# Kernel optimization log

Measured on AMD Instinct MI355X. Metric: run time of the kernel, lower is better.

The kernel has to match this reference:

```python
import jax, jax.numpy as jnp
import numpy as np

EPS = 1e-5
K = 20


def _edge_layer(feat, W, g, b, k):
    # feat: (B, N, C). Dynamic KNN in feature space (DGCNN get_graph_feature).
    B = feat.shape[0]
    inner = jnp.einsum('bnc,bmc->bnm', feat, feat)          # (B,N,N)
    xx = jnp.sum(feat * feat, axis=-1)                      # (B,N)
    neg_dist = 2.0 * inner - xx[:, :, None] - xx[:, None, :]
    idx = jax.lax.top_k(neg_dist, k)[1]                     # (B,N,k) nearest (incl self)
    nbr = feat[jnp.arange(B)[:, None, None], idx]           # (B,N,k,C) gather
    ctr = jnp.broadcast_to(feat[:, :, None, :], nbr.shape)
    edge = jnp.concatenate([nbr - ctr, ctr], axis=-1)       # (B,N,k,2C)
    h = jnp.einsum('bnke,oe->bnko', edge, W)                # 1x1 conv
    mean = jnp.mean(h, axis=(0, 1, 2))
    var = jnp.var(h, axis=(0, 1, 2))                        # biased, as torch BN training
    h = (h - mean) * jax.lax.rsqrt(var + EPS) * g + b
    h = jax.nn.leaky_relu(h, 0.2)
    return jnp.max(h, axis=2)                               # max over k -> (B,N,C)


def setup_inputs() -> dict:
    key = jax.random.key(0)
    ks = jax.random.split(key, 8)
    B, N, C, OUT = 16, 2048, 64, 1024
    d = {
        'x': jax.random.normal(ks[0], (B, N, C), jnp.float32),
        'W1': jax.random.normal(ks[1], (C, 2 * C), jnp.float32) * 0.05,
        'g1': jnp.ones((C,), jnp.float32), 'b1': jnp.zeros((C,), jnp.float32),
        'W2': jax.random.normal(ks[2], (C, 2 * C), jnp.float32) * 0.05,
        'g2': jnp.ones((C,), jnp.float32), 'b2': jnp.zeros((C,), jnp.float32),
        'W3': jax.random.normal(ks[3], (C, 2 * C), jnp.float32) * 0.05,
        'g3': jnp.ones((C,), jnp.float32), 'b3': jnp.zeros((C,), jnp.float32),
        'Wf': jax.random.normal(ks[4], (OUT, 3 * C), jnp.float32) * 0.05,
        'gf': jnp.ones((OUT,), jnp.float32), 'bf': jnp.zeros((OUT,), jnp.float32),
    }
    return d


def reference(x, W1, g1, b1, W2, g2, b2, W3, g3, b3, Wf, gf, bf):
    # x: (B, N, C)
    f1 = _edge_layer(x, W1, g1, b1, K)
    f2 = _edge_layer(f1, W2, g2, b2, K)
    f3 = _edge_layer(f2, W3, g3, b3, K)
    cat = jnp.concatenate([f1, f2, f3], axis=-1)            # (B,N,3C)
    h = jnp.einsum('bnc,oc->bno', cat, Wf)                  # 1x1 conv1d
    mean = jnp.mean(h, axis=(0, 1))
    var = jnp.var(h, axis=(0, 1))
    h = (h - mean) * jax.lax.rsqrt(var + EPS) * gf + bf
    h = jax.nn.leaky_relu(h, 0.2)
    return jnp.max(h, axis=1)                               # global max over N -> (B,OUT)
```

## Files before the change

kernel.cpp:

```cpp
#include <hip/hip_runtime.h>

#define BB 16
#define NN 2048
#define CC 64
#define KNN 20
#define OUTC 1024

__global__ __launch_bounds__(256) void xx32_kernel(const float* __restrict__ F,
                                                   float* __restrict__ xxf) {
  int p = blockIdx.x * 256 + threadIdx.x;
  const float* f = F + (size_t)p * CC;
  float t[64];
#pragma unroll
  for (int c = 0; c < 64; ++c) t[c] = f[c] * f[c];
  float r[8];
#pragma unroll
  for (int j = 0; j < 8; ++j) r[j] = t[j];
#pragma unroll
  for (int i = 8; i < 64; i += 8)
#pragma unroll
    for (int j = 0; j < 8; ++j) r[j] += t[i + j];
  float res = ((r[0] + r[1]) + (r[2] + r[3])) + ((r[4] + r[5]) + (r[6] + r[7]));
  xxf[p] = res;
}

__device__ __forceinline__ unsigned long long packkey(float s, int m) {
  unsigned int u = __float_as_uint(s);
  u ^= (u >> 31) ? 0xFFFFFFFFu : 0x80000000u;
  return ((unsigned long long)u << 32) | (unsigned int)(NN - 1 - m);
}

#define INSERT_KEY(key)                                   \
  if ((key) > kv[KNN - 1]) {                              \
    _Pragma("unroll")                                     \
    for (int jj = KNN - 1; jj >= 1; --jj) {               \
      if ((key) > kv[jj - 1]) kv[jj] = kv[jj - 1];        \
      else if ((key) > kv[jj]) kv[jj] = (key);            \
    }                                                     \
    if ((key) > kv[0]) kv[0] = (key);                     \
  }

__global__ __launch_bounds__(256) void knn_fast(const float* __restrict__ F,
                                                const float* __restrict__ xxf,
                                                int* __restrict__ idx) {
  __shared__ __align__(16) char smem[52736];
  float* SQc = (float*)smem;
  float* SPc = (float*)(smem + 17408);
  float* SS  = (float*)(smem + 34816);
  float* xq  = (float*)(smem + 52224);
  float* xp  = (float*)(smem + 52480);

  int b = blockIdx.y, n0 = blockIdx.x * 64, t = threadIdx.x;
  const float* fb = F + (size_t)b * NN * CC;

#pragma unroll
  for (int j = 0; j < 4; ++j) {
    int v = t + 256 * j;
    int row = v >> 4, c4 = (v & 15) * 4;
    float4 val = *(const float4*)(fb + (size_t)(n0 + row) * CC + c4);
    SQc[(c4 + 0) * 68 + row] = val.x;
    SQc[(c4 + 1) * 68 + row] = val.y;
    SQc[(c4 + 2) * 68 + row] = val.z;
    SQc[(c4 + 3) * 68 + row] = val.w;
  }
  if (t < 64) xq[t] = xxf[b * NN + n0 + t];

  unsigned long long kv[KNN];
#pragma unroll
  for (int k = 0; k < KNN; ++k) kv[k] = 0ull;

  int tx = t & 15, ty = t >> 4;
  int r = t & 63, qq = t >> 6;

  for (int m0 = 0; m0 < NN; m0 += 64) {
    __syncthreads();
#pragma unroll
    for (int j = 0; j < 4; ++j) {
      int v = t + 256 * j;
      int row = v >> 4, c4 = (v & 15) * 4;
      float4 val = *(const float4*)(fb + (size_t)(m0 + row) * CC + c4);
      SPc[(c4 + 0) * 68 + row] = val.x;
      SPc[(c4 + 1) * 68 + row] = val.y;
      SPc[(c4 + 2) * 68 + row] = val.z;
      SPc[(c4 + 3) * 68 + row] = val.w;
    }
    if (t < 64) xp[t] = xxf[b * NN + m0 + t];
    __syncthreads();

    float acc[4][4] = {};
#pragma unroll 8
    for (int c = 0; c < 64; ++c) {
      float4 av = *(const float4*)&SQc[c * 68 + ty * 4];
      float4 bv = *(const float4*)&SPc[c * 68 + tx * 4];
      float a[4] = {av.x, av.y, av.z, av.w};
      float bb4[4] = {bv.x, bv.y, bv.z, bv.w};
#pragma unroll
      for (int i = 0; i < 4; ++i)
#pragma unroll
        for (int j = 0; j < 4; ++j) acc[i][j] = fmaf(a[i], bb4[j], acc[i][j]);
    }
#pragma unroll
    for (int i = 0; i < 4; ++i) {
      float xn = xq[ty * 4 + i];
      float4 sv;
      sv.x = (2.0f * acc[i][0] - xn) - xp[tx * 4 + 0];
      sv.y = (2.0f * acc[i][1] - xn) - xp[tx * 4 + 1];
      sv.z = (2.0f * acc[i][2] - xn) - xp[tx * 4 + 2];
      sv.w = (2.0f * acc[i][3] - xn) - xp[tx * 4 + 3];
      *(float4*)&SS[(ty * 4 + i) * 68 + tx * 4] = sv;
    }
    __syncthreads();

#pragma unroll
    for (int j4 = 0; j4 < 4; ++j4) {
      float4 sv = *(const float4*)&SS[r * 68 + qq * 16 + j4 * 4];
      int mb = m0 + qq * 16 + j4 * 4;
      unsigned long long k0 = packkey(sv.x, mb + 0);
      INSERT_KEY(k0)
      unsigned long long k1 = packkey(sv.y, mb + 1);
      INSERT_KEY(k1)
      unsigned long long k2 = packkey(sv.z, mb + 2);
      INSERT_KEY(k2)
      unsigned long long k3 = packkey(sv.w, mb + 3);
      INSERT_KEY(k3)
    }
  }

  __syncthreads();
  unsigned long long* keys = (unsigned long long*)smem;
#pragma unroll
  for (int k = 0; k < KNN; ++k) keys[t * KNN + k] = kv[k];
  __syncthreads();
  if (t < 64) {
    for (int q2 = 1; q2 < 4; ++q2) {
      int base = (q2 * 64 + t) * KNN;
#pragma unroll 1
      for (int k = 0; k < KNN; ++k) {
        unsigned long long key = keys[base + k];
        if (key <= kv[KNN - 1]) break;
        INSERT_KEY(key)
      }
    }
    int* dst = idx + (size_t)(b * NN + n0 + t) * KNN;
#pragma unroll
    for (int k = 0; k < KNN; ++k)
      dst[k] = (NN - 1) - (int)(unsigned int)(kv[k] & 0xFFFFFFFFull);
  }
}

template <int CACHE>
__global__ __launch_bounds__(256) void stats_k(const float* __restrict__ F,
                                               const float* __restrict__ W,
                                               const int* __restrict__ idx,
                                               double* __restrict__ sums,
                                               float* __restrict__ hout) {
  __shared__ float Fn[64 * 64];
  __shared__ double rs[256], rss[256];
  int b = blockIdx.y, n0 = blockIdx.x * 64, t = threadIdx.x;
  int o = t & 63, g4 = t >> 6;
#pragma unroll
  for (int j = 0; j < 4; ++j) {
    int v = t + 256 * j;
    int row = v >> 4, c4 = (v & 15) * 4;
    *(float4*)&Fn[row * 64 + c4] =
        *(const float4*)(F + ((size_t)(b * NN + n0 + row)) * CC + c4);
  }
  float4 w0[16], w1[16];
  const float* wp = W + o * 128;
#pragma unroll
  for (int c4 = 0; c4 < 16; ++c4) {
    w0[c4] = *(const float4*)(wp + c4 * 4);
    w1[c4] = *(const float4*)(wp + 64 + c4 * 4);
  }
  __syncthreads();
  double s = 0.0, ss = 0.0;
  for (int i = 0; i < 16; ++i) {
    int n = n0 + g4 * 16 + i;
    float4 fn[16];
#pragma unroll
    for (int c4 = 0; c4 < 16; ++c4) fn[c4] = *(float4*)&Fn[(g4 * 16 + i) * 64 + c4 * 4];
    const int* ip = idx + ((size_t)(b * NN + n)) * KNN;
#pragma unroll 1
    for (int k = 0; k < KNN; k += 2) {
      const float* fp0 = F + ((size_t)(b * NN + ip[k])) * CC;
      const float* fp1 = F + ((size_t)(b * NN + ip[k + 1])) * CC;
      float a0 = 0.f, a1 = 0.f;
#pragma unroll
      for (int c4 = 0; c4 < 16; ++c4) {
        float4 f0 = *(const float4*)(fp0 + c4 * 4);
        float4 f1 = *(const float4*)(fp1 + c4 * 4);
        float4 fv = fn[c4], wv = w0[c4];
        a0 = fmaf(wv.x, f0.x - fv.x, a0);
        a0 = fmaf(wv.y, f0.y - fv.y, a0);
        a0 = fmaf(wv.z, f0.z - fv.z, a0);
        a0 = fmaf(wv.w, f0.w - fv.w, a0);
        a1 = fmaf(wv.x, f1.x - fv.x, a1);
        a1 = fmaf(wv.y, f1.y - fv.y, a1);
        a1 = fmaf(wv.z, f1.z - fv.z, a1);
        a1 = fmaf(wv.w, f1.w - fv.w, a1);
      }
#pragma unroll
      for (int c4 = 0; c4 < 16; ++c4) {
        float4 fv = fn[c4], wv = w1[c4];
        a0 = fmaf(wv.x, fv.x, a0);
        a0 = fmaf(wv.y, fv.y, a0);
        a0 = fmaf(wv.z, fv.z, a0);
        a0 = fmaf(wv.w, fv.w, a0);
        a1 = fmaf(wv.x, fv.x, a1);
        a1 = fmaf(wv.y, fv.y, a1);
        a1 = fmaf(wv.z, fv.z, a1);
        a1 = fmaf(wv.w, fv.w, a1);
      }
      s += (double)a0 + (double)a1;
      ss += (double)a0 * (double)a0 + (double)a1 * (double)a1;
      if (CACHE) {
        float* hp = hout + (((size_t)(b * NN + n)) * KNN + k) * 64 + o;
        hp[0] = a0;
        hp[64] = a1;
      }
    }
  }
  rs[t] = s; rss[t] = ss;
  __syncthreads();
  if (t < 64) {
    double a = rs[t] + rs[t + 64] + rs[t + 128] + rs[t + 192];
    double q = rss[t] + rss[t + 64] + rss[t + 128] + rss[t + 192];
    atomicAdd(&sums[o], a);
    atomicAdd(&sums[64 + o], q);
  }
}

__global__ void finalize_np(const double* __restrict__ sums, double cntinv,
                            float* __restrict__ mrs) {
  int c = threadIdx.x;
  double mean = sums[c] * cntinv;
  double var = sums[64 + c] * cntinv - mean * mean;
  mrs[c] = (float)mean;
  mrs[64 + c] = 1.0f / sqrtf((float)var + 1e-5f);
}

__global__ __launch_bounds__(256) void apply_cached(const float* __restrict__ hin,
                                                    const float* __restrict__ mrs,
                                                    const float* __restrict__ gv,
                                                    const float* __restrict__ bvv,
                                                    float* __restrict__ Fo) {
  int t = threadIdx.x;
  int o = t & 63, ng = t >> 6;
  size_t n = (size_t)blockIdx.x * 4 + ng;
  const float* hp = hin + n * KNN * 64 + o;
  float m32 = mrs[o], rs32 = mrs[64 + o];
  float gg = gv[o], bb = bvv[o];
  float mx = -3.0e38f;
#pragma unroll
  for (int k = 0; k < KNN; ++k) {
    float h = hp[k * 64];
    float d = h - m32;
    d = d * rs32;
    d = d * gg;
    float y = d + bb;
    y = y >= 0.f ? y : 0.2f * y;
    mx = fmaxf(mx, y);
  }
  Fo[n * 64 + o] = mx;
}

__global__ __launch_bounds__(256) void apply_rec(const float* __restrict__ F,
                                                 const float* __restrict__ W,
                                                 const int* __restrict__ idx,
                                                 const float* __restrict__ mrs,
                                                 const float* __restrict__ gv,
                                                 const float* __restrict__ bvv,
                                                 float* __restrict__ Fo) {
  __shared__ float Fn[64 * 64];
  int b = blockIdx.y, n0 = blockIdx.x * 64, t = threadIdx.x;
  int o = t & 63, g4 = t >> 6;
#pragma unroll
  for (int j = 0; j < 4; ++j) {
    int v = t + 256 * j;
    int row = v >> 4, c4 = (v & 15) * 4;
    *(float4*)&Fn[row * 64 + c4] =
        *(const float4*)(F + ((size_t)(b * NN + n0 + row)) * CC + c4);
  }
  float4 w0[16], w1[16];
  const float* wp = W + o * 128;
#pragma unroll
  for (int c4 = 0; c4 < 16; ++c4) {
    w0[c4] = *(const float4*)(wp + c4 * 4);
    w1[c4] = *(const float4*)(wp + 64 + c4 * 4);
  }
  __syncthreads();
  float m32 = mrs[o], rs32 = mrs[64 + o];
  float gg = gv[o], bb = bvv[o];
  for (int i = 0; i < 16; ++i) {
    int n = n0 + g4 * 16 + i;
    float4 fn[16];
#pragma unroll
    for (int c4 = 0; c4 < 16; ++c4) fn[c4] = *(float4*)&Fn[(g4 * 16 + i) * 64 + c4 * 4];
    const int* ip = idx + ((size_t)(b * NN + n)) * KNN;
    float mx = -3.0e38f;
#pragma unroll 1
    for (int k = 0; k < KNN; k += 2) {
      const float* fp0 = F + ((size_t)(b * NN + ip[k])) * CC;
      const float* fp1 = F + ((size_t)(b * NN + ip[k + 1])) * CC;
      float a0 = 0.f, a1 = 0.f;
#pragma unroll
      for (int c4 = 0; c4 < 16; ++c4) {
        float4 f0 = *(const float4*)(fp0 + c4 * 4);
        float4 f1 = *(const float4*)(fp1 + c4 * 4);
        float4 fv = fn[c4], wv = w0[c4];
        a0 = fmaf(wv.x, f0.x - fv.x, a0);
        a0 = fmaf(wv.y, f0.y - fv.y, a0);
        a0 = fmaf(wv.z, f0.z - fv.z, a0);
        a0 = fmaf(wv.w, f0.w - fv.w, a0);
        a1 = fmaf(wv.x, f1.x - fv.x, a1);
        a1 = fmaf(wv.y, f1.y - fv.y, a1);
        a1 = fmaf(wv.z, f1.z - fv.z, a1);
        a1 = fmaf(wv.w, f1.w - fv.w, a1);
      }
#pragma unroll
      for (int c4 = 0; c4 < 16; ++c4) {
        float4 fv = fn[c4], wv = w1[c4];
        a0 = fmaf(wv.x, fv.x, a0);
        a0 = fmaf(wv.y, fv.y, a0);
        a0 = fmaf(wv.z, fv.z, a0);
        a0 = fmaf(wv.w, fv.w, a0);
        a1 = fmaf(wv.x, fv.x, a1);
        a1 = fmaf(wv.y, fv.y, a1);
        a1 = fmaf(wv.z, fv.z, a1);
        a1 = fmaf(wv.w, fv.w, a1);
      }
      float d0 = a0 - m32; d0 = d0 * rs32; d0 = d0 * gg;
      float y0 = d0 + bb;
      y0 = y0 >= 0.f ? y0 : 0.2f * y0;
      float d1 = a1 - m32; d1 = d1 * rs32; d1 = d1 * gg;
      float y1 = d1 + bb;
      y1 = y1 >= 0.f ? y1 : 0.2f * y1;
      mx = fmaxf(mx, fmaxf(y0, y1));
    }
    Fo[((size_t)(b * NN + n)) * CC + o] = mx;
  }
}

template <int CACHE>
__global__ __launch_bounds__(256) void fstats_split(const float* __restrict__ F1,
                                                    const float* __restrict__ F2,
                                                    const float* __restrict__ F3,
                                                    const float* __restrict__ Wf,
                                                    double* __restrict__ sums,
                                                    float* __restrict__ hout) {
  __shared__ float Wl[64 * 193];
  __shared__ double rs[256], rss[256];
  int b = blockIdx.y, o0 = blockIdx.x * 64, t = threadIdx.x;
  int nbase = blockIdx.z * (NN / 8);
  for (int j = 0; j < 48; ++j) {
    int v = t + 256 * j;
    int oo = v / 192, c = v - oo * 192;
    Wl[oo * 193 + c] = Wf[(size_t)(o0 + oo) * 192 + c];
  }
  __syncthreads();
  int o = t & 63, g = t >> 6;
  const float* fs[3] = {F1, F2, F3};
  double s = 0.0, ss = 0.0;
  for (int n0 = nbase; n0 < nbase + NN / 8; n0 += 16) {
    int n = n0 + g * 4;
    float h[4] = {0.f, 0.f, 0.f, 0.f};
#pragma unroll
    for (int part = 0; part < 3; ++part) {
      const float* src = fs[part] + ((size_t)(b * NN + n)) * CC;
      const float* wp = &Wl[o * 193 + part * 64];
#pragma unroll 4
      for (int c4 = 0; c4 < 16; ++c4) {
        float4 w4 = {wp[c4 * 4], wp[c4 * 4 + 1], wp[c4 * 4 + 2], wp[c4 * 4 + 3]};
#pragma unroll
        for (int i = 0; i < 4; ++i) {
          float4 v = *(const float4*)(src + (size_t)i * CC + c4 * 4);
          h[i] = fmaf(w4.x, v.x, h[i]);
          h[i] = fmaf(w4.y, v.y, h[i]);
          h[i] = fmaf(w4.z, v.z, h[i]);
          h[i] = fmaf(w4.w, v.w, h[i]);
        }
      }
    }
#pragma unroll
    for (int i = 0; i < 4; ++i) {
      s += (double)h[i];
      ss += (double)h[i] * (double)h[i];
      if (CACHE) hout[((size_t)(b * NN + n + i)) * OUTC + o0 + o] = h[i];
    }
  }
  rs[t] = s; rss[t] = ss;
  __syncthreads();
  if (t < 64) {
    double a = rs[t] + rs[t + 64] + rs[t + 128] + rs[t + 192];
    double q = rss[t] + rss[t + 64] + rss[t + 128] + rss[t + 192];
    atomicAdd(&sums[o0 + o], a);
    atomicAdd(&sums[1024 + o0 + o], q);
  }
}

__global__ void finalize_f(const double* __restrict__ sums,
                           const float* __restrict__ g,
                           const float* __restrict__ bb, double cntinv,
                           float* __restrict__ scsh) {
  int c = blockIdx.x * 256 + threadIdx.x;
  double mean = sums[c] * cntinv;
  double var = sums[1024 + c] * cntinv - mean * mean;
  double sc = (double)g[c] / sqrt(var + 1e-5);
  scsh[c] = (float)sc;
  scsh[1024 + c] = (float)((double)bb[c] - mean * sc);
}

__global__ __launch_bounds__(256) void fapply_stream(const float* __restrict__ hin,
                                                     const float* __restrict__ scsh,
                                                     float* __restrict__ pmax) {
  int b = blockIdx.y, t = threadIdx.x;
  int o = blockIdx.x * 256 + t;
  int nbase = blockIdx.z * (NN / 8);
  float sc = scsh[o], sh = scsh[1024 + o];
  float mx = -3.0e38f;
  const float* hp = hin + ((size_t)(b * NN + nbase)) * OUTC + o;
#pragma unroll 4
  for (int n = 0; n < NN / 8; ++n) {
    float y = fmaf(sc, hp[(size_t)n * OUTC], sh);
    y = y >= 0.f ? y : 0.2f * y;
    mx = fmaxf(mx, y);
  }
  pmax[((size_t)blockIdx.z * BB + b) * OUTC + o] = mx;
}

__global__ __launch_bounds__(256) void freduce(const float* __restrict__ pmax,
                                               float* __restrict__ out) {
  int v = blockIdx.x * 256 + threadIdx.x;
  float mx = -3.0e38f;
#pragma unroll
  for (int ch = 0; ch < 8; ++ch) mx = fmaxf(mx, pmax[(size_t)ch * BB * OUTC + v]);
  out[v] = mx;
}

__global__ __launch_bounds__(256) void fapply32(const float* __restrict__ F1,
                                                const float* __restrict__ F2,
                                                const float* __restrict__ F3,
                                                const float* __restrict__ Wf,
                                                const float* __restrict__ scsh,
                                                float* __restrict__ out) {
  __shared__ float Wl[64 * 193];
  __shared__ float redm[4][64];
  int b = blockIdx.y, o0 = blockIdx.x * 64, t = threadIdx.x;
  for (int j = 0; j < 48; ++j) {
    int v = t + 256 * j;
    int oo = v / 192, c = v - oo * 192;
    Wl[oo * 193 + c] = Wf[(size_t)(o0 + oo) * 192 + c];
  }
  __syncthreads();
  int o = t & 63, g = t >> 6;
  float sc = scsh[o0 + o], sh = scsh[1024 + o0 + o];
  const float* fs[3] = {F1, F2, F3};
  float mx = -3.0e38f;
  for (int n0 = 0; n0 < NN; n0 += 16) {
    int n = n0 + g * 4;
    float h[4] = {0.f, 0.f, 0.f, 0.f};
#pragma unroll
    for (int part = 0; part < 3; ++part) {
      const float* src = fs[part] + ((size_t)(b * NN + n)) * CC;
      const float* wp = &Wl[o * 193 + part * 64];
#pragma unroll 4
      for (int c4 = 0; c4 < 16; ++c4) {
        float4 w4 = {wp[c4 * 4], wp[c4 * 4 + 1], wp[c4 * 4 + 2], wp[c4 * 4 + 3]};
#pragma unroll
        for (int i = 0; i < 4; ++i) {
          float4 v = *(const float4*)(src + (size_t)i * CC + c4 * 4);
          h[i] = fmaf(w4.x, v.x, h[i]);
          h[i] = fmaf(w4.y, v.y, h[i]);
          h[i] = fmaf(w4.z, v.z, h[i]);
          h[i] = fmaf(w4.w, v.w, h[i]);
        }
      }
    }
#pragma unroll
    for (int i = 0; i < 4; ++i) {
      float y = fmaf(sc, h[i], sh);
      y = y >= 0.f ? y : 0.2f * y;
      mx = fmaxf(mx, y);
    }
  }
  redm[g][o] = mx;
  __syncthreads();
  if (t < 64) {
    float m = fmaxf(fmaxf(redm[0][o], redm[1][o]), fmaxf(redm[2][o], redm[3][o]));
    out[(size_t)b * OUTC + o0 + o] = m;
  }
}

extern "C" void kernel_launch(void* const* d_in, const int* in_sizes, int n_in,
                              void* d_out, int out_size, void* d_ws, size_t ws_size,
                              hipStream_t stream) {
  (void)in_sizes; (void)n_in; (void)out_size;
  const float* x  = (const float*)d_in[0];
  const float* W1 = (const float*)d_in[1];
  const float* g1 = (const float*)d_in[2];
  const float* b1 = (const float*)d_in[3];
  const float* W2 = (const float*)d_in[4];
  const float* g2 = (const float*)d_in[5];
  const float* b2 = (const float*)d_in[6];
  const float* W3 = (const float*)d_in[7];
  const float* g3 = (const float*)d_in[8];
  const float* b3 = (const float*)d_in[9];
  const float* Wf = (const float*)d_in[10];
  const float* gf = (const float*)d_in[11];
  const float* bf = (const float*)d_in[12];
  float* out = (float*)d_out;

  char* wsb = (char*)d_ws;
  float* F1f    = (float*)(wsb + 0);
  float* F2f    = (float*)(wsb + 8388608);
  float* F3f    = (float*)(wsb + 16777216);
  float* xxf    = (float*)(wsb + 25165824);
  int* idx      = (int*)(wsb + 25296896);
  double* sumsd = (double*)(wsb + 27918336);
  double* fsums = (double*)(wsb + 27920384);
  float* fscsh  = (float*)(wsb + 27936768);
  float* mrs    = (float*)(wsb + 27944960);
  float* pmax   = (float*)(wsb + 27945984);
  float* hbuf   = (float*)(wsb + 29360128);
  const bool cache = ws_size >= (size_t)29360128 + (size_t)BB * NN * KNN * 64 * 4;

  const float* Fin[3] = {x, F1f, F2f};
  float* Fout[3] = {F1f, F2f, F3f};
  const float* Ws[3] = {W1, W2, W3};
  const float* gs[3] = {g1, g2, g3};
  const float* bs[3] = {b1, b2, b3};

  for (int L = 0; L < 3; ++L) {
    xx32_kernel<<<dim3(BB * NN / 256), 256, 0, stream>>>(Fin[L], xxf);
    knn_fast<<<dim3(NN / 64, BB), 256, 0, stream>>>(Fin[L], xxf, idx);
    hipMemsetAsync(sumsd, 0, 128 * sizeof(double), stream);
    if (cache)
      stats_k<1><<<dim3(NN / 64, BB), 256, 0, stream>>>(Fin[L], Ws[L], idx, sumsd, hbuf);
    else
      stats_k<0><<<dim3(NN / 64, BB), 256, 0, stream>>>(Fin[L], Ws[L], idx, sumsd, nullptr);
    finalize_np<<<1, 64, 0, stream>>>(sumsd, 1.0 / (double)(BB * NN * KNN), mrs);
    if (cache)
      apply_cached<<<dim3(BB * NN / 4), 256, 0, stream>>>(hbuf, mrs, gs[L], bs[L], Fout[L]);
    else
      apply_rec<<<dim3(NN / 64, BB), 256, 0, stream>>>(Fin[L], Ws[L], idx, mrs,
                                                       gs[L], bs[L], Fout[L]);
  }
  hipMemsetAsync(fsums, 0, 2048 * sizeof(double), stream);
  if (cache) {
    fstats_split<1><<<dim3(OUTC / 64, BB, 8), 256, 0, stream>>>(F1f, F2f, F3f, Wf,
                                                                fsums, hbuf);
    finalize_f<<<4, 256, 0, stream>>>(fsums, gf, bf, 1.0 / (double)(BB * NN), fscsh);
    fapply_stream<<<dim3(OUTC / 256, BB, 8), 256, 0, stream>>>(hbuf, fscsh, pmax);
    freduce<<<dim3(BB * OUTC / 256), 256, 0, stream>>>(pmax, out);
  } else {
    fstats_split<0><<<dim3(OUTC / 64, BB, 8), 256, 0, stream>>>(F1f, F2f, F3f, Wf,
                                                                fsums, nullptr);
    finalize_f<<<4, 256, 0, stream>>>(fsums, gf, bf, 1.0 / (double)(BB * NN), fscsh);
    fapply32<<<dim3(OUTC / 64, BB), 256, 0, stream>>>(F1f, F2f, F3f, Wf, fscsh, out);
  }
}
```

Measured before the change: 3.085 ms.

## Rewrite final conv stats kernel as shared-memory tiled GEMM with 4x4 register blocking

Replaces the final 1x1 conv statistics kernel, which streamed features from global memory per output channel, with a 64x64 output-tiled GEMM. Feature and weight chunks are staged transposed in shared memory, and each thread accumulates a 4x4 register block. This raises arithmetic intensity and cuts redundant global loads of the features. Per-channel double sums are reduced in shared memory before the atomics, but there are now many more blocks issuing atomics (512 row tiles per channel group), and the transposed shared-memory stores may hit bank conflicts.

```diff
diff --git a/kernel.cpp b/kernel.cpp
--- a/kernel.cpp
+++ b/kernel.cpp
@@ -342,59 +342,89 @@
 }
 
 template <int CACHE>
-__global__ __launch_bounds__(256) void fstats_split(const float* __restrict__ F1,
-                                                    const float* __restrict__ F2,
-                                                    const float* __restrict__ F3,
-                                                    const float* __restrict__ Wf,
-                                                    double* __restrict__ sums,
-                                                    float* __restrict__ hout) {
-  __shared__ float Wl[64 * 193];
-  __shared__ double rs[256], rss[256];
-  int b = blockIdx.y, o0 = blockIdx.x * 64, t = threadIdx.x;
-  int nbase = blockIdx.z * (NN / 8);
-  for (int j = 0; j < 48; ++j) {
-    int v = t + 256 * j;
-    int oo = v / 192, c = v - oo * 192;
-    Wl[oo * 193 + c] = Wf[(size_t)(o0 + oo) * 192 + c];
-  }
-  __syncthreads();
-  int o = t & 63, g = t >> 6;
+__global__ __launch_bounds__(256) void fstats_gemm(const float* __restrict__ F1,
+                                                   const float* __restrict__ F2,
+                                                   const float* __restrict__ F3,
+                                                   const float* __restrict__ Wf,
+                                                   double* __restrict__ sums,
+                                                   float* __restrict__ hout) {
+  __shared__ __align__(16) char smem[34816];
+  float* Ft = (float*)smem;
+  float* Wt = (float*)(smem + 17408);
+  int o0 = blockIdx.x * 64;
+  int r0 = blockIdx.y * 64;
+  int t = threadIdx.x;
+  int to = t & 15, tn = t >> 4;
   const float* fs[3] = {F1, F2, F3};
-  double s = 0.0, ss = 0.0;
-  for (int n0 = nbase; n0 < nbase + NN / 8; n0 += 16) {
-    int n = n0 + g * 4;
-    float h[4] = {0.f, 0.f, 0.f, 0.f};
-#pragma unroll
-    for (int part = 0; part < 3; ++part) {
-      const float* src = fs[part] + ((size_t)(b * NN + n)) * CC;
-      const float* wp = &Wl[o * 193 + part * 64];
-#pragma unroll 4
-      for (int c4 = 0; c4 < 16; ++c4) {
-        float4 w4 = {wp[c4 * 4], wp[c4 * 4 + 1], wp[c4 * 4 + 2], wp[c4 * 4 + 3]};
-#pragma unroll
-        for (int i = 0; i < 4; ++i) {
-          float4 v = *(const float4*)(src + (size_t)i * CC + c4 * 4);
-          h[i] = fmaf(w4.x, v.x, h[i]);
-          h[i] = fmaf(w4.y, v.y, h[i]);
-          h[i] = fmaf(w4.z, v.z, h[i]);
-          h[i] = fmaf(w4.w, v.w, h[i]);
-        }
-      }
-    }
+
+  float acc[4][4] = {};
+#pragma unroll 1
+  for (int ch = 0; ch < 3; ++ch) {
+    __syncthreads();
+#pragma unroll
+    for (int j = 0; j < 16; ++j) {
+      int v = t + 256 * j;
+      int oo = v >> 6, c = v & 63;
+      Wt[c * 68 + oo] = Wf[(size_t)(o0 + oo) * 192 + ch * 64 + c];
+    }
+#pragma unroll
+    for (int j = 0; j < 4; ++j) {
+      int v = t + 256 * j;
+      int row = v >> 4, c4 = (v & 15) * 4;
+      float4 val = *(const float4*)(fs[ch] + ((size_t)(r0 + row)) * CC + c4);
+      Ft[(c4 + 0) * 68 + row] = val.x;
+      Ft[(c4 + 1) * 68 + row] = val.y;
+      Ft[(c4 + 2) * 68 + row] = val.z;
+      Ft[(c4 + 3) * 68 + row] = val.w;
+    }
+    __syncthreads();
+#pragma unroll 8
+    for (int c = 0; c < 64; ++c) {
+      float4 av = *(const float4*)&Ft[c * 68 + tn * 4];
+      float4 wv = *(const float4*)&Wt[c * 68 + to * 4];
+      float a[4] = {av.x, av.y, av.z, av.w};
+      float w[4] = {wv.x, wv.y, wv.z, wv.w};
+#pragma unroll
+      for (int i = 0; i < 4; ++i)
+#pragma unroll
+        for (int j = 0; j < 4; ++j) acc[i][j] = fmaf(a[i], w[j], acc[i][j]);
+    }
+  }
+  if (CACHE) {
 #pragma unroll
     for (int i = 0; i < 4; ++i) {
-      s += (double)h[i];
-      ss += (double)h[i] * (double)h[i];
-      if (CACHE) hout[((size_t)(b * NN + n + i)) * OUTC + o0 + o] = h[i];
-    }
-  }
-  rs[t] = s; rss[t] = ss;
+      float4 hv = {acc[i][0], acc[i][1], acc[i][2], acc[i][3]};
+      *(float4*)&hout[((size_t)(r0 + tn * 4 + i)) * OUTC + o0 + to * 4] = hv;
+    }
+  }
+  double sj[4], ssj[4];
+#pragma unroll
+  for (int j = 0; j < 4; ++j) {
+    sj[j] = 0.0; ssj[j] = 0.0;
+#pragma unroll
+    for (int i = 0; i < 4; ++i) {
+      sj[j] += (double)acc[i][j];
+      ssj[j] += (double)acc[i][j] * (double)acc[i][j];
+    }
+  }
+  __syncthreads();
+  double* reds = (double*)smem;
+  double* redss = (double*)(smem + 8192);
+#pragma unroll
+  for (int j = 0; j < 4; ++j) {
+    reds[(to * 4 + j) * 16 + tn] = sj[j];
+    redss[(to * 4 + j) * 16 + tn] = ssj[j];
+  }
   __syncthreads();
   if (t < 64) {
-    double a = rs[t] + rs[t + 64] + rs[t + 128] + rs[t + 192];
-    double q = rss[t] + rss[t + 64] + rss[t + 128] + rss[t + 192];
-    atomicAdd(&sums[o0 + o], a);
-    atomicAdd(&sums[1024 + o0 + o], q);
+    double s = 0.0, ss = 0.0;
+#pragma unroll
+    for (int u = 0; u < 16; ++u) {
+      s += reds[t * 16 + u];
+      ss += redss[t * 16 + u];
+    }
+    atomicAdd(&sums[o0 + t], s);
+    atomicAdd(&sums[1024 + o0 + t], ss);
   }
 }
 
@@ -547,14 +577,14 @@
   }
   hipMemsetAsync(fsums, 0, 2048 * sizeof(double), stream);
   if (cache) {
-    fstats_split<1><<<dim3(OUTC / 64, BB, 8), 256, 0, stream>>>(F1f, F2f, F3f, Wf,
-                                                                fsums, hbuf);
+    fstats_gemm<1><<<dim3(OUTC / 64, BB * NN / 64), 256, 0, stream>>>(F1f, F2f, F3f,
+                                                                      Wf, fsums, hbuf);
     finalize_f<<<4, 256, 0, stream>>>(fsums, gf, bf, 1.0 / (double)(BB * NN), fscsh);
     fapply_stream<<<dim3(OUTC / 256, BB, 8), 256, 0, stream>>>(hbuf, fscsh, pmax);
     freduce<<<dim3(BB * OUTC / 256), 256, 0, stream>>>(pmax, out);
   } else {
-    fstats_split<0><<<dim3(OUTC / 64, BB, 8), 256, 0, stream>>>(F1f, F2f, F3f, Wf,
-                                                                fsums, nullptr);
+    fstats_gemm<0><<<dim3(OUTC / 64, BB * NN / 64), 256, 0, stream>>>(F1f, F2f, F3f,
+                                                                      Wf, fsums, nullptr);
     finalize_f<<<4, 256, 0, stream>>>(fsums, gf, bf, 1.0 / (double)(BB * NN), fscsh);
     fapply32<<<dim3(OUTC / 64, BB), 256, 0, stream>>>(F1f, F2f, F3f, Wf, fscsh, out);
   }
```

Result: faster. 2.617 ms (-15.2%).
